# Performance work log

Hardware: AMD Instinct MI355X
Metric: run time of the kernel (lower is better)

Reference implementation:

```python
import jax, jax.numpy as jnp
import numpy as np

N_EMBEDS = 1024
N_HEADS = 16
EPS = 1e-3


def layer_norm(x, gamma, beta):
    mean = jnp.mean(x, axis=-1, keepdims=True)
    var = jnp.mean((x - mean) ** 2, axis=-1, keepdims=True)
    return gamma * (x - mean) / jnp.sqrt(var + EPS) + beta


def setup_inputs() -> dict:
    key = jax.random.key(0)
    ks = jax.random.split(key, 8)
    B, T, C = 4, 2048, N_EMBEDS
    s = 1.0 / np.sqrt(C)
    return {
        "x": jax.random.normal(ks[0], (B, T, C), dtype=jnp.float32),
        "w_qkv": jax.random.normal(ks[1], (C, 3 * C), dtype=jnp.float32) * s,
        "w_proj": jax.random.normal(ks[2], (C, C), dtype=jnp.float32) * s,
        "b_proj": jnp.zeros((C,), dtype=jnp.float32),
        "w1": jax.random.normal(ks[3], (C, 4 * C), dtype=jnp.float32) * s,
        "b1": jnp.zeros((4 * C,), dtype=jnp.float32),
        "w2": jax.random.normal(ks[4], (4 * C, C), dtype=jnp.float32) * (0.5 / np.sqrt(C)),
        "b2": jnp.zeros((C,), dtype=jnp.float32),
        "gamma1": jnp.ones((C,), dtype=jnp.float32),
        "beta1": jnp.zeros((C,), dtype=jnp.float32),
        "gamma2": jnp.ones((C,), dtype=jnp.float32),
        "beta2": jnp.zeros((C,), dtype=jnp.float32),
    }


def reference(x, w_qkv, w_proj, b_proj, w1, b1, w2, b2, gamma1, beta1, gamma2, beta2):
    B, T, C = x.shape
    H = N_HEADS
    D = C // H
    scale = D ** -0.5

    # --- attention sub-layer (pre-LN) ---
    h = layer_norm(x, gamma1, beta1)
    qkv = h @ w_qkv                      # [B,T,3C]
    q, k, v = jnp.split(qkv, 3, axis=-1)
    q = q.reshape(B, T, H, D).transpose(0, 2, 1, 3)  # [B,H,T,D]
    k = k.reshape(B, T, H, D).transpose(0, 2, 1, 3)
    v = v.reshape(B, T, H, D).transpose(0, 2, 1, 3)
    att = jnp.einsum('bhqd,bhkd->bhqk', q, k) * scale
    causal = jnp.tril(jnp.ones((T, T), dtype=bool))
    att = jnp.where(causal[None, None], att, jnp.float32(-1e9))
    att = jax.nn.softmax(att, axis=-1)
    out = jnp.einsum('bhqk,bhkd->bhqd', att, v)
    out = out.transpose(0, 2, 1, 3).reshape(B, T, C)
    x = x + out @ w_proj + b_proj

    # --- FFN sub-layer (pre-LN, erf-GELU) ---
    h = layer_norm(x, gamma2, beta2)
    h = jax.nn.gelu(h @ w1 + b1, approximate=False)
    x = x + h @ w2 + b2
    return x
```

## Files before the change

### kernel.cpp

```cpp
#include <hip/hip_runtime.h>
#include <hip/hip_bf16.h>
#include <cstdint>
#include <cstddef>

#define B_ 4
#define T_ 2048
#define C_ 1024
#define H_ 16
#define D_ 64
#define M_ (B_*T_)

using bf16_t = __hip_bfloat16;
typedef __bf16 v8bf __attribute__((ext_vector_type(8)));
typedef float  v4f  __attribute__((ext_vector_type(4)));
typedef float  f32x16 __attribute__((ext_vector_type(16)));

#define QSCALE (0.125f * 1.44269504088896340736f)

static __device__ __forceinline__ bf16_t f2bf(float v){ return __float2bfloat16(v); }

static __device__ __forceinline__ void glds16(const bf16_t* g, bf16_t* l){
  __builtin_amdgcn_global_load_lds((__attribute__((address_space(1))) void*)g,
                                   (__attribute__((address_space(3))) void*)l, 16, 0, 0);
}

static __device__ __forceinline__ uint32_t cvt_pk_bf16(float lo, float hi){
  uint32_t w;
  asm("v_cvt_pk_bf16_f32 %0, %1, %2" : "=v"(w) : "v"(lo), "v"(hi));
  return w;
}

__global__ void k_transpose_cast(const float* __restrict__ in, bf16_t* __restrict__ out,
                                 int K, int N){
  __shared__ float tile[32][33];
  int k0 = blockIdx.y*32, n0 = blockIdx.x*32;
  int tx = threadIdx.x, ty = threadIdx.y;
  #pragma unroll
  for(int j=0;j<32;j+=8) tile[ty+j][tx] = in[(size_t)(k0+ty+j)*N + n0+tx];
  __syncthreads();
  #pragma unroll
  for(int j=0;j<32;j+=8) out[(size_t)(n0+ty+j)*K + k0+tx] = f2bf(tile[tx][ty+j]);
}

__global__ __launch_bounds__(256) void k_layernorm(const float* __restrict__ x,
                                                   const float* __restrict__ gamma,
                                                   const float* __restrict__ beta,
                                                   bf16_t* __restrict__ out){
  int row = blockIdx.x;
  int tid = threadIdx.x;
  const float4 v = reinterpret_cast<const float4*>(x + (size_t)row*C_)[tid];
  float s  = v.x+v.y+v.z+v.w;
  float ss = v.x*v.x+v.y*v.y+v.z*v.z+v.w*v.w;
  #pragma unroll
  for(int m=1;m<64;m<<=1){ s += __shfl_xor(s,m); ss += __shfl_xor(ss,m); }
  __shared__ float sbuf[4], ssbuf[4];
  int wid = tid>>6, lane = tid&63;
  if(lane==0){ sbuf[wid]=s; ssbuf[wid]=ss; }
  __syncthreads();
  s  = sbuf[0]+sbuf[1]+sbuf[2]+sbuf[3];
  ss = ssbuf[0]+ssbuf[1]+ssbuf[2]+ssbuf[3];
  float mean = s * (1.0f/C_);
  float var  = ss * (1.0f/C_) - mean*mean;
  float rstd = rsqrtf(var + 1e-3f);
  const float4 g = reinterpret_cast<const float4*>(gamma)[tid];
  const float4 b = reinterpret_cast<const float4*>(beta)[tid];
  union { ushort4 u; bf16_t h[4]; } pk;
  pk.h[0] = f2bf(g.x*(v.x-mean)*rstd + b.x);
  pk.h[1] = f2bf(g.y*(v.y-mean)*rstd + b.y);
  pk.h[2] = f2bf(g.z*(v.z-mean)*rstd + b.z);
  pk.h[3] = f2bf(g.w*(v.w-mean)*rstd + b.w);
  *reinterpret_cast<ushort4*>(out + (size_t)row*C_ + tid*4) = pk.u;
}

template<int MODE>
__global__ __launch_bounds__(512, 1)
void k_gemm8(const bf16_t* __restrict__ A, const bf16_t* __restrict__ Bt,
             const float* __restrict__ bias, const float* resid,
             void* out0, void* out1, void* out2,
             int N, int K, int gx)
{
  __shared__ __align__(16) bf16_t As[2][256*64];
  __shared__ __align__(16) bf16_t Bs[3][128*64];
  const int tid = threadIdx.x, lane = tid & 63, w = tid >> 6;
  const int wm = w >> 1, wn = w & 1;

  const int nwg = gx * 32;
  const int orig = blockIdx.y * gx + blockIdx.x;
  const int swz = (orig & 7) * (nwg >> 3) + (orig >> 3);
  const int ct = swz % gx, rt = swz / gx;
  const int row0 = rt * 256, col0 = ct * 128;

  const int sswz = ((lane & 7) ^ ((lane >> 3) & 7)) * 8;
  const int srow = w * 8 + (lane >> 3);
  const bf16_t* Agb = A  + (size_t)(row0 + srow) * K + sswz;
  const bf16_t* Bgb = Bt + (size_t)(col0 + srow) * K + sswz;

  auto stageA = [&](int tt){
    const bf16_t* src = Agb + tt * 64;
    bf16_t* dst = &As[tt & 1][w * 512];
    #pragma unroll
    for (int i = 0; i < 4; ++i)
      glds16(src + (size_t)(i*64) * K, dst + i*4096);
  };
  auto stageB = [&](int tt){
    const bf16_t* src = Bgb + tt * 64;
    bf16_t* dst = &Bs[tt % 3][w * 512];
    #pragma unroll
    for (int i = 0; i < 2; ++i)
      glds16(src + (size_t)(i*64) * K, dst + i*4096);
  };

  v8bf af[4][2], bfv[4][2];
  v4f acc[4][4] = {};

  auto LDA = [&](int ab){
    const bf16_t* base = &As[ab][0];
    #pragma unroll
    for (int m = 0; m < 4; ++m)
      #pragma unroll
      for (int kk = 0; kk < 2; ++kk) {
        const int r  = wm*64 + m*16 + (lane & 15);
        const int sl = (kk*4 + (lane >> 4)) ^ (lane & 7);
        af[m][kk] = *reinterpret_cast<const v8bf*>(base + r*64 + sl*8);
      }
  };
  auto LDB = [&](int bb, int nh){
    const bf16_t* base = &Bs[bb][0];
    #pragma unroll
    for (int n = 0; n < 2; ++n)
      #pragma unroll
      for (int kk = 0; kk < 2; ++kk) {
        const int r  = wn*64 + (nh*2+n)*16 + (lane & 15);
        const int sl = (kk*4 + (lane >> 4)) ^ (lane & 7);
        bfv[nh*2+n][kk] = *reinterpret_cast<const v8bf*>(base + r*64 + sl*8);
      }
  };

#define MFMA_Q(nh_) \
  __builtin_amdgcn_s_setprio(1); \
  _Pragma("unroll") \
  for (int kk = 0; kk < 2; ++kk) \
    _Pragma("unroll") \
    for (int m = 0; m < 4; ++m) \
      _Pragma("unroll") \
      for (int n = 0; n < 2; ++n) \
        acc[m][(nh_)*2+n] = __builtin_amdgcn_mfma_f32_16x16x32_bf16( \
            af[m][kk], bfv[(nh_)*2+n][kk], acc[m][(nh_)*2+n], 0,0,0); \
  __builtin_amdgcn_s_setprio(0);

#define BAR()   __builtin_amdgcn_s_barrier()
#define LGKM0() do { asm volatile("s_waitcnt lgkmcnt(0)" ::: "memory"); \
                     __builtin_amdgcn_sched_barrier(0); } while(0)
#define VM6()   asm volatile("s_waitcnt vmcnt(6)" ::: "memory")
#define VM0()   asm volatile("s_waitcnt vmcnt(0)" ::: "memory")

  const int NT = K >> 6;
  const int NP = NT >> 1;

  stageB(0); stageA(0); stageB(1); stageA(1);
  VM6();
  BAR();

  for (int j = 0; j < NP; ++j) {
    const int t0 = 2*j, t1 = 2*j + 1, t2 = 2*j + 2, t3 = 2*j + 3;
    const bool more = (j + 1 < NP);
    LDA(0); LDB(t0 % 3, 0);
    if (more) stageB(t2);
    BAR(); LGKM0(); MFMA_Q(0); BAR();
    LDB(t0 % 3, 1);
    if (more) { stageA(t2); VM6(); } else { VM0(); }
    BAR(); LGKM0(); MFMA_Q(1); BAR();
    LDA(1); LDB(t1 % 3, 0);
    if (more) stageB(t3);
    BAR(); LGKM0(); MFMA_Q(0); BAR();
    LDB(t1 % 3, 1);
    if (more) { stageA(t3); VM6(); } else { VM0(); }
    BAR(); LGKM0(); MFMA_Q(1); BAR();
  }
#undef MFMA_Q
#undef BAR
#undef LGKM0
#undef VM6
#undef VM0

  #pragma unroll
  for (int mf = 0; mf < 4; ++mf) {
    const int rbase = row0 + wm*64 + mf*16 + (lane>>4)*4;
    #pragma unroll
    for (int nf = 0; nf < 4; ++nf) {
      const int c = col0 + wn*64 + nf*16 + (lane&15);
      #pragma unroll
      for (int i = 0; i < 4; ++i) {
        const int rr = rbase + i;
        float v = acc[mf][nf][i];
        if constexpr(MODE==0){
          const int sec = c >> 10, cc = c & 1023;
          const int h = cc >> 6, d = cc & 63;
          const int b = rr >> 11, t = rr & 2047;
          if(sec==0)      ((bf16_t*)out0)[((size_t)(b*H_ + h)*T_ + t)*D_ + d] = f2bf(v * QSCALE);
          else if(sec==1) ((bf16_t*)out1)[((size_t)(b*H_ + h)*T_ + t)*D_ + d] = f2bf(v);
          else            ((bf16_t*)out2)[((size_t)(b*H_ + h)*D_ + d)*T_ + t] = f2bf(v);
        } else if constexpr(MODE==1){
          ((float*)out0)[(size_t)rr*N + c] = v + bias[c] + resid[(size_t)rr*N + c];
        } else if constexpr(MODE==2){
          float o = v + bias[c];
          o = 0.5f*o*(1.0f + erff(o*0.70710678118f));
          ((bf16_t*)out0)[(size_t)rr*N + c] = f2bf(o);
        } else {
          ((float*)out0)[(size_t)rr*N + c] = v + bias[c] + resid[(size_t)rr*N + c];
        }
      }
    }
  }
}

__global__ __launch_bounds__(256)
void k_attn(const bf16_t* __restrict__ Q, const bf16_t* __restrict__ Kg,
            const bf16_t* __restrict__ Vt, bf16_t* __restrict__ O)
{
  __shared__ __align__(16) bf16_t Ks [64][72];
  __shared__ __align__(16) bf16_t Vts[64][72];
  __shared__ __align__(16) bf16_t Os [128][72];
  const int bh = blockIdx.y;
  const int pair = blockIdx.x;
  const int tid = threadIdx.x, lane = tid & 63, w = tid >> 6;
  const int ql = lane & 31, hi = lane >> 5;
  const int srow = tid >> 2;
  const int scol = (tid & 3) * 16;
  const bf16_t* Kgp = Kg + ((size_t)bh*T_ + srow)*D_ + scol;
  const bf16_t* Vtp = Vt + ((size_t)bh*D_ + srow)*T_ + scol;
  const int b = bh >> 4, h = bh & 15;

  for(int half=0; half<2; ++half){
    const int qt = half ? pair : (15 - pair);
    const int qbase = qt*128 + w*32;
    const int q = qbase + ql;

    v8bf qf[4];
    {
      const bf16_t* Qb = Q + ((size_t)bh*T_ + q)*D_ + hi*8;
      #pragma unroll
      for(int ds=0; ds<4; ds++)
        qf[ds] = *reinterpret_cast<const v8bf*>(Qb + ds*16);
    }

    f32x16 accO[2] = {};
    float mrun = -1e30f, lrun = 0.0f;
    const int NT = (qt + 1) * 2;

    v8bf kr0 = *reinterpret_cast<const v8bf*>(Kgp);
    v8bf kr1 = *reinterpret_cast<const v8bf*>(Kgp + 8);
    v8bf vr0 = *reinterpret_cast<const v8bf*>(Vtp);
    v8bf vr1 = *reinterpret_cast<const v8bf*>(Vtp + 8);

    for(int t=0; t<NT; t++){
      const int kv0 = t*64;
      *reinterpret_cast<v8bf*>(&Ks [srow][scol  ]) = kr0;
      *reinterpret_cast<v8bf*>(&Ks [srow][scol+8]) = kr1;
      *reinterpret_cast<v8bf*>(&Vts[srow][scol  ]) = vr0;
      *reinterpret_cast<v8bf*>(&Vts[srow][scol+8]) = vr1;
      __syncthreads();
      if(t+1 < NT){
        const size_t kn = (size_t)(kv0 + 64);
        kr0 = *reinterpret_cast<const v8bf*>(Kgp + kn*D_);
        kr1 = *reinterpret_cast<const v8bf*>(Kgp + kn*D_ + 8);
        vr0 = *reinterpret_cast<const v8bf*>(Vtp + kn);
        vr1 = *reinterpret_cast<const v8bf*>(Vtp + kn + 8);
      }

      if(kv0 <= qbase + 31){
        f32x16 sT[2] = {};
        #pragma unroll
        for(int kvh=0; kvh<2; kvh++)
          #pragma unroll
          for(int ds=0; ds<4; ds++){
            v8bf kf = *reinterpret_cast<const v8bf*>(&Ks[kvh*32 + ql][ds*16 + hi*8]);
            sT[kvh] = __builtin_amdgcn_mfma_f32_32x32x16_bf16(kf, qf[ds], sT[kvh], 0,0,0);
          }

        if(kv0 + 63 > qbase){
          const int qrel = q - kv0 - hi*4;
          #pragma unroll
          for(int kvh=0; kvh<2; kvh++)
            #pragma unroll
            for(int r=0; r<16; r++){
              const int c = kvh*32 + (r&3) + 8*(r>>2);
              if(c > qrel) sT[kvh][r] = -1e30f;
            }
        }

        float pm = sT[0][0];
        #pragma unroll
        for(int r=1; r<16; r++) pm = fmaxf(pm, sT[0][r]);
        #pragma unroll
        for(int r=0; r<16; r++) pm = fmaxf(pm, sT[1][r]);
        pm = fmaxf(pm, __shfl_xor(pm, 32));

        if(__any(pm - mrun > 8.0f)){
          const float mnew = fmaxf(mrun, pm);
          const float corr = __builtin_amdgcn_exp2f(mrun - mnew);
          mrun = mnew;
          lrun *= corr;
          #pragma unroll
          for(int dh=0; dh<2; dh++)
            #pragma unroll
            for(int r=0; r<16; r++) accO[dh][r] *= corr;
        }

        float rs = 0.0f;
        #pragma unroll
        for(int kvh=0; kvh<2; kvh++)
          #pragma unroll
          for(int r=0; r<16; r++){
            float p = __builtin_amdgcn_exp2f(sT[kvh][r] - mrun);
            sT[kvh][r] = p;
            rs += p;
          }
        rs += __shfl_xor(rs, 32);
        lrun += rs;

        v8bf pfrag[4];
        #pragma unroll
        for(int s4=0; s4<4; s4++){
          const int kvh = s4>>1, bb = (s4&1)*8;
          uint32_t wa = cvt_pk_bf16(sT[kvh][bb+0], sT[kvh][bb+1]);
          uint32_t wb = cvt_pk_bf16(sT[kvh][bb+2], sT[kvh][bb+3]);
          uint32_t wc = cvt_pk_bf16(sT[kvh][bb+4], sT[kvh][bb+5]);
          uint32_t wd = cvt_pk_bf16(sT[kvh][bb+6], sT[kvh][bb+7]);
          uint32_t xwa = (uint32_t)__shfl_xor((int)wa, 32);
          uint32_t xwb = (uint32_t)__shfl_xor((int)wb, 32);
          uint32_t xwc = (uint32_t)__shfl_xor((int)wc, 32);
          uint32_t xwd = (uint32_t)__shfl_xor((int)wd, 32);
          union { uint32_t u[4]; v8bf v; } pk;
          pk.u[0] = hi ? xwc : wa;
          pk.u[1] = hi ? xwd : wb;
          pk.u[2] = hi ? wc  : xwa;
          pk.u[3] = hi ? wd  : xwb;
          pfrag[s4] = pk.v;
        }

        #pragma unroll
        for(int dh=0; dh<2; dh++)
          #pragma unroll
          for(int s4=0; s4<4; s4++){
            v8bf vf = *reinterpret_cast<const v8bf*>(&Vts[dh*32 + ql][s4*16 + hi*8]);
            accO[dh] = __builtin_amdgcn_mfma_f32_32x32x16_bf16(vf, pfrag[s4], accO[dh], 0,0,0);
          }
      }
      __syncthreads();
    }

    const float inv = 1.0f / lrun;
    #pragma unroll
    for(int dh=0; dh<2; dh++)
      #pragma unroll
      for(int rg=0; rg<4; rg++){
        uint32_t lo_ = cvt_pk_bf16(accO[dh][rg*4+0]*inv, accO[dh][rg*4+1]*inv);
        uint32_t hi_ = cvt_pk_bf16(accO[dh][rg*4+2]*inv, accO[dh][rg*4+3]*inv);
        uint2 w2; w2.x = lo_; w2.y = hi_;
        *reinterpret_cast<uint2*>(&Os[w*32 + ql][dh*32 + rg*8 + hi*4]) = w2;
      }
    __syncthreads();
    const int orow = tid >> 1, ocol = (tid & 1) * 32;
    bf16_t* Og = O + ((size_t)(b*T_ + qt*128 + orow))*C_ + h*64 + ocol;
    #pragma unroll
    for(int j=0;j<4;j++)
      *reinterpret_cast<v8bf*>(Og + j*8) = *reinterpret_cast<const v8bf*>(&Os[orow][ocol + j*8]);
    __syncthreads();
  }
}

extern "C" void kernel_launch(void* const* d_in, const int* in_sizes, int n_in,
                              void* d_out, int out_size, void* d_ws, size_t ws_size,
                              hipStream_t stream) {
  const float* x      = (const float*)d_in[0];
  const float* w_qkv  = (const float*)d_in[1];
  const float* w_proj = (const float*)d_in[2];
  const float* b_proj = (const float*)d_in[3];
  const float* w1     = (const float*)d_in[4];
  const float* b1     = (const float*)d_in[5];
  const float* w2     = (const float*)d_in[6];
  const float* b2     = (const float*)d_in[7];
  const float* gamma1 = (const float*)d_in[8];
  const float* beta1  = (const float*)d_in[9];
  const float* gamma2 = (const float*)d_in[10];
  const float* beta2  = (const float*)d_in[11];

  char* ws = (char*)d_ws;
  bf16_t* wqkv_t  = (bf16_t*)(ws + 0);
  bf16_t* wproj_t = (bf16_t*)(ws + 6291456);
  bf16_t* w1_t    = (bf16_t*)(ws + 8388608);
  bf16_t* w2_t    = (bf16_t*)(ws + 16777216);
  bf16_t* qb      = (bf16_t*)(ws + 25165824);
  bf16_t* kb      = (bf16_t*)(ws + 41943040);
  bf16_t* vtb     = (bf16_t*)(ws + 58720256);
  bf16_t* obuf    = (bf16_t*)(ws + 75497472);
  bf16_t* hb      = (bf16_t*)(ws + 92274688);
  bf16_t* gb      = (bf16_t*)(ws + 25165824);
  float*  x2      = (float*)d_out;

  dim3 tb(32,8);
  k_transpose_cast<<<dim3(3072/32, 1024/32), tb, 0, stream>>>(w_qkv,  wqkv_t, 1024, 3072);
  k_transpose_cast<<<dim3(1024/32, 1024/32), tb, 0, stream>>>(w_proj, wproj_t,1024, 1024);
  k_transpose_cast<<<dim3(4096/32, 1024/32), tb, 0, stream>>>(w1,     w1_t,   1024, 4096);
  k_transpose_cast<<<dim3(1024/32, 4096/32), tb, 0, stream>>>(w2,     w2_t,   4096, 1024);

  k_layernorm<<<M_, 256, 0, stream>>>(x, gamma1, beta1, hb);

  k_gemm8<0><<<dim3(24, 32), 512, 0, stream>>>(hb, wqkv_t, nullptr, nullptr,
                                               qb, kb, vtb, 3072, 1024, 24);
  k_attn<<<dim3(8, B_*H_), 256, 0, stream>>>(qb, kb, vtb, obuf);

  k_gemm8<1><<<dim3(8, 32), 512, 0, stream>>>(obuf, wproj_t, b_proj, x,
                                              x2, nullptr, nullptr, 1024, 1024, 8);
  k_layernorm<<<M_, 256, 0, stream>>>(x2, gamma2, beta2, hb);

  k_gemm8<2><<<dim3(32, 32), 512, 0, stream>>>(hb, w1_t, b1, nullptr,
                                               gb, nullptr, nullptr, 4096, 1024, 32);
  k_gemm8<3><<<dim3(8, 32), 512, 0, stream>>>(gb, w2_t, b2, x2,
                                              d_out, nullptr, nullptr, 1024, 4096, 8);
}
```

Measured before the change: 419.0 us.

## Use 256x256 GEMM tiles and split-K for FFN down projection

Adds a new GEMM kernel with 256x256 output tiles (8 waves arranged 2x4) and uses it for the QKV and FFN-up projections, which raises arithmetic intensity per LDS load. The FFN-down GEMM is split along K into two halves that write bf16 partial sums, and a separate elementwise kernel adds both partials, the bias and the residual. This fills more CUs with the larger tiles, at the cost of extra partial-sum traffic, an additional launch, and bf16 rounding of the partials. The old GEMM kernel is kept only for the attention output projection.

After: 404.8 us. 3.4% less time.

```diff
diff --git a/kernel.cpp b/kernel.cpp
--- a/kernel.cpp
+++ b/kernel.cpp
@@ -18,6 +18,9 @@
 #define QSCALE (0.125f * 1.44269504088896340736f)
 
 static __device__ __forceinline__ bf16_t f2bf(float v){ return __float2bfloat16(v); }
+static __device__ __forceinline__ float bfraw2f(unsigned short u){
+  union { unsigned int i; float f; } c; c.i = ((unsigned int)u) << 16; return c.f;
+}
 
 static __device__ __forceinline__ void glds16(const bf16_t* g, bf16_t* l){
   __builtin_amdgcn_global_load_lds((__attribute__((address_space(1))) void*)g,
@@ -72,12 +75,170 @@
   *reinterpret_cast<ushort4*>(out + (size_t)row*C_ + tid*4) = pk.u;
 }
 
+__global__ __launch_bounds__(256)
+void k_add2(const bf16_t* __restrict__ p0, const bf16_t* __restrict__ p1,
+            const float* __restrict__ bias, float* out){
+  const int row = blockIdx.x, tid = threadIdx.x;
+  float4 xr = reinterpret_cast<const float4*>(out + (size_t)row*C_)[tid];
+  const ushort4 a = reinterpret_cast<const ushort4*>(p0 + (size_t)row*C_)[tid];
+  const ushort4 b = reinterpret_cast<const ushort4*>(p1 + (size_t)row*C_)[tid];
+  const float4 g = reinterpret_cast<const float4*>(bias)[tid];
+  xr.x += bfraw2f(a.x) + bfraw2f(b.x) + g.x;
+  xr.y += bfraw2f(a.y) + bfraw2f(b.y) + g.y;
+  xr.z += bfraw2f(a.z) + bfraw2f(b.z) + g.z;
+  xr.w += bfraw2f(a.w) + bfraw2f(b.w) + g.w;
+  reinterpret_cast<float4*>(out + (size_t)row*C_)[tid] = xr;
+}
+
 template<int MODE>
+__global__ __launch_bounds__(512, 1)
+void k_gemm9(const bf16_t* __restrict__ A, const bf16_t* __restrict__ Bt,
+             const float* __restrict__ bias, const float* resid,
+             void* out0, void* out1, void* out2,
+             int N, int ld, int klen, int gx)
+{
+  __shared__ __align__(16) bf16_t As[2][2][128*64];
+  __shared__ __align__(16) bf16_t Bs[2][2][128*64];
+  const int tid = threadIdx.x, lane = tid & 63, w = tid >> 6;
+  const int wm = w >> 2, wn = w & 3;
+
+  const int nwg = gx * 32;
+  const int orig = blockIdx.y * gx + blockIdx.x;
+  const int swz = (orig & 7) * (nwg >> 3) + (orig >> 3);
+  const int ct = swz % gx, rt = swz / gx;
+  const int row0 = rt * 256, col0 = ct * 256;
+  const int koff = blockIdx.z * klen;
+
+  const int sswz = ((lane & 7) ^ ((lane >> 3) & 7)) * 8;
+  const int srow = w * 8 + (lane >> 3);
+  const bf16_t* Agb = A  + (size_t)(row0 + srow) * ld + koff + sswz;
+  const bf16_t* Bgb = Bt + (size_t)(col0 + srow) * ld + koff + sswz;
+
+  auto stageA = [&](int tt, int hh){
+    const bf16_t* src = Agb + (size_t)(hh * 128) * ld + tt * 64;
+    bf16_t* dst = &As[tt & 1][hh][w * 512];
+    glds16(src, dst);
+    glds16(src + (size_t)64 * ld, dst + 4096);
+  };
+  auto stageB = [&](int tt, int hh){
+    const bf16_t* src = Bgb + (size_t)(hh * 128) * ld + tt * 64;
+    bf16_t* dst = &Bs[tt & 1][hh][w * 512];
+    glds16(src, dst);
+    glds16(src + (size_t)64 * ld, dst + 4096);
+  };
+
+  v8bf af[4][2], bfv[4][2];
+  v4f acc[8][4] = {};
+
+  auto LDA = [&](int bb, int mh){
+    const bf16_t* base = &As[bb][wm][0];
+    #pragma unroll
+    for (int m = 0; m < 4; ++m)
+      #pragma unroll
+      for (int kk = 0; kk < 2; ++kk) {
+        const int r  = mh*64 + m*16 + (lane & 15);
+        const int sl = (kk*4 + (lane >> 4)) ^ (lane & 7);
+        af[m][kk] = *reinterpret_cast<const v8bf*>(base + r*64 + sl*8);
+      }
+  };
+  auto LDB = [&](int bb){
+    const bf16_t* base = &Bs[bb][wn >> 1][0];
+    #pragma unroll
+    for (int n = 0; n < 4; ++n)
+      #pragma unroll
+      for (int kk = 0; kk < 2; ++kk) {
+        const int r  = (wn & 1)*64 + n*16 + (lane & 15);
+        const int sl = (kk*4 + (lane >> 4)) ^ (lane & 7);
+        bfv[n][kk] = *reinterpret_cast<const v8bf*>(base + r*64 + sl*8);
+      }
+  };
+
+#define MFMA_Q(mh_, nh_) \
+  __builtin_amdgcn_s_setprio(1); \
+  _Pragma("unroll") \
+  for (int kk = 0; kk < 2; ++kk) \
+    _Pragma("unroll") \
+    for (int m = 0; m < 4; ++m) \
+      _Pragma("unroll") \
+      for (int n = 0; n < 2; ++n) \
+        acc[(mh_)*4+m][(nh_)*2+n] = __builtin_amdgcn_mfma_f32_16x16x32_bf16( \
+            af[m][kk], bfv[(nh_)*2+n][kk], acc[(mh_)*4+m][(nh_)*2+n], 0,0,0); \
+  __builtin_amdgcn_s_setprio(0);
+
+#define BAR()   __builtin_amdgcn_s_barrier()
+#define LGKM0() do { asm volatile("s_waitcnt lgkmcnt(0)" ::: "memory"); \
+                     __builtin_amdgcn_sched_barrier(0); } while(0)
+
+  stageA(0,0); stageA(0,1); stageB(0,0); stageB(0,1);
+  stageB(1,0); stageB(1,1); stageA(1,0);
+  asm volatile("s_waitcnt vmcnt(6)" ::: "memory");
+  BAR();
+
+  const int NP = (klen >> 6) >> 1;
+  for (int j = 0; j < NP; ++j) {
+    const int t2 = 2*j + 2, t3 = 2*j + 3;
+    const bool more = (j + 1 < NP);
+    LDA(0, 0); LDB(0);
+    stageA(2*j + 1, 1);
+    BAR(); LGKM0(); MFMA_Q(0, 0); BAR();
+    if (more) stageB(t2, 0);
+    BAR(); MFMA_Q(0, 1); BAR();
+    LDA(0, 1);
+    if (more) stageB(t2, 1);
+    BAR(); LGKM0(); MFMA_Q(1, 0); BAR();
+    if (more) { stageA(t2, 0); asm volatile("s_waitcnt vmcnt(6)" ::: "memory"); }
+    else      {                asm volatile("s_waitcnt vmcnt(0)" ::: "memory"); }
+    BAR(); MFMA_Q(1, 1); BAR();
+    LDA(1, 0); LDB(1);
+    if (more) stageA(t2, 1);
+    BAR(); LGKM0(); MFMA_Q(0, 0); BAR();
+    if (more) stageB(t3, 0);
+    BAR(); MFMA_Q(0, 1); BAR();
+    LDA(1, 1);
+    if (more) stageB(t3, 1);
+    BAR(); LGKM0(); MFMA_Q(1, 0); BAR();
+    if (more) { stageA(t3, 0); asm volatile("s_waitcnt vmcnt(6)" ::: "memory"); }
+    else      {                asm volatile("s_waitcnt vmcnt(0)" ::: "memory"); }
+    BAR(); MFMA_Q(1, 1); BAR();
+  }
+#undef MFMA_Q
+#undef BAR
+#undef LGKM0
+
+  #pragma unroll
+  for (int mf = 0; mf < 8; ++mf) {
+    const int rbase = row0 + wm*128 + mf*16 + (lane>>4)*4;
+    #pragma unroll
+    for (int nf = 0; nf < 4; ++nf) {
+      const int c = col0 + wn*64 + nf*16 + (lane&15);
+      #pragma unroll
+      for (int i = 0; i < 4; ++i) {
+        const int rr = rbase + i;
+        float v = acc[mf][nf][i];
+        if constexpr(MODE==0){
+          const int sec = c >> 10, cc = c & 1023;
+          const int h = cc >> 6, d = cc & 63;
+          const int b = rr >> 11, t = rr & 2047;
+          if(sec==0)      ((bf16_t*)out0)[((size_t)(b*H_ + h)*T_ + t)*D_ + d] = f2bf(v * QSCALE);
+          else if(sec==1) ((bf16_t*)out1)[((size_t)(b*H_ + h)*T_ + t)*D_ + d] = f2bf(v);
+          else            ((bf16_t*)out2)[((size_t)(b*H_ + h)*D_ + d)*T_ + t] = f2bf(v);
+        } else if constexpr(MODE==2){
+          float o = v + bias[c];
+          o = 0.5f*o*(1.0f + erff(o*0.70710678118f));
+          ((bf16_t*)out0)[(size_t)rr*N + c] = f2bf(o);
+        } else {
+          bf16_t* dst = blockIdx.z ? (bf16_t*)out1 : (bf16_t*)out0;
+          dst[(size_t)rr*N + c] = f2bf(v);
+        }
+      }
+    }
+  }
+}
+
 __global__ __launch_bounds__(512, 1)
 void k_gemm8(const bf16_t* __restrict__ A, const bf16_t* __restrict__ Bt,
              const float* __restrict__ bias, const float* resid,
-             void* out0, void* out1, void* out2,
-             int N, int K, int gx)
+             float* out0, int N, int K, int gx)
 {
   __shared__ __align__(16) bf16_t As[2][256*64];
   __shared__ __align__(16) bf16_t Bs[3][128*64];
@@ -154,9 +315,7 @@
 #define VM6()   asm volatile("s_waitcnt vmcnt(6)" ::: "memory")
 #define VM0()   asm volatile("s_waitcnt vmcnt(0)" ::: "memory")
 
-  const int NT = K >> 6;
-  const int NP = NT >> 1;
-
+  const int NP = (K >> 6) >> 1;
   stageB(0); stageA(0); stageB(1); stageA(1);
   VM6();
   BAR();
@@ -192,23 +351,7 @@
       #pragma unroll
       for (int i = 0; i < 4; ++i) {
         const int rr = rbase + i;
-        float v = acc[mf][nf][i];
-        if constexpr(MODE==0){
-          const int sec = c >> 10, cc = c & 1023;
-          const int h = cc >> 6, d = cc & 63;
-          const int b = rr >> 11, t = rr & 2047;
-          if(sec==0)      ((bf16_t*)out0)[((size_t)(b*H_ + h)*T_ + t)*D_ + d] = f2bf(v * QSCALE);
-          else if(sec==1) ((bf16_t*)out1)[((size_t)(b*H_ + h)*T_ + t)*D_ + d] = f2bf(v);
-          else            ((bf16_t*)out2)[((size_t)(b*H_ + h)*D_ + d)*T_ + t] = f2bf(v);
-        } else if constexpr(MODE==1){
-          ((float*)out0)[(size_t)rr*N + c] = v + bias[c] + resid[(size_t)rr*N + c];
-        } else if constexpr(MODE==2){
-          float o = v + bias[c];
-          o = 0.5f*o*(1.0f + erff(o*0.70710678118f));
-          ((bf16_t*)out0)[(size_t)rr*N + c] = f2bf(o);
-        } else {
-          ((float*)out0)[(size_t)rr*N + c] = v + bias[c] + resid[(size_t)rr*N + c];
-        }
+        out0[(size_t)rr*N + c] = acc[mf][nf][i] + bias[c] + resid[(size_t)rr*N + c];
       }
     }
   }
@@ -407,16 +550,17 @@
 
   k_layernorm<<<M_, 256, 0, stream>>>(x, gamma1, beta1, hb);
 
-  k_gemm8<0><<<dim3(24, 32), 512, 0, stream>>>(hb, wqkv_t, nullptr, nullptr,
-                                               qb, kb, vtb, 3072, 1024, 24);
+  k_gemm9<0><<<dim3(12, 32, 1), 512, 0, stream>>>(hb, wqkv_t, nullptr, nullptr,
+                                                  qb, kb, vtb, 3072, 1024, 1024, 12);
   k_attn<<<dim3(8, B_*H_), 256, 0, stream>>>(qb, kb, vtb, obuf);
 
-  k_gemm8<1><<<dim3(8, 32), 512, 0, stream>>>(obuf, wproj_t, b_proj, x,
-                                              x2, nullptr, nullptr, 1024, 1024, 8);
+  k_gemm8<<<dim3(8, 32), 512, 0, stream>>>(obuf, wproj_t, b_proj, x,
+                                           x2, 1024, 1024, 8);
   k_layernorm<<<M_, 256, 0, stream>>>(x2, gamma2, beta2, hb);
 
-  k_gemm8<2><<<dim3(32, 32), 512, 0, stream>>>(hb, w1_t, b1, nullptr,
-                                               gb, nullptr, nullptr, 4096, 1024, 32);
-  k_gemm8<3><<<dim3(8, 32), 512, 0, stream>>>(gb, w2_t, b2, x2,
-                                              d_out, nullptr, nullptr, 1024, 4096, 8);
-}
+  k_gemm9<2><<<dim3(16, 32, 1), 512, 0, stream>>>(hb, w1_t, b1, nullptr,
+                                                  gb, nullptr, nullptr, 4096, 1024, 1024, 16);
+  k_gemm9<4><<<dim3(4, 32, 2), 512, 0, stream>>>(gb, w2_t, nullptr, nullptr,
+                                                 obuf, hb, nullptr, 1024, 4096, 2048, 4);
+  k_add2<<<M_, 256, 0, stream>>>(obuf, hb, b2, x2);
+}
```
